# Kernel optimization log

Hardware: AMD Instinct MI355X
Metric: run time of the kernel (lower is better)

Reference implementation:

```python
import jax, jax.numpy as jnp
import numpy as np

NENTITY = 200000
NRELATION = 500
HIDDEN = 256
GAMMA = 12.0
EPS = 2.0
EMB_RANGE = (GAMMA + EPS) / HIDDEN


def setup_inputs() -> dict:
    key = jax.random.key(0)
    ks = jax.random.split(key, 8)
    B, NEG = 256, 1024
    head = jax.random.randint(ks[0], (B, 1), 0, NENTITY)
    tail = jax.random.randint(ks[1], (B, NEG), 0, NENTITY)
    relation = jax.random.randint(ks[2], (B,), 0, NRELATION)
    entity_emb = jax.random.uniform(ks[3], (NENTITY, HIDDEN), jnp.float32, -EMB_RANGE, EMB_RANGE)
    relation_emb = jax.random.uniform(ks[4], (NRELATION, 2 * HIDDEN), jnp.float32, -EMB_RANGE, EMB_RANGE)
    lim = 1.0 / np.sqrt(2 * HIDDEN)
    W_fc = jax.random.uniform(ks[5], (HIDDEN, 2 * HIDDEN), jnp.float32, -lim, lim)
    b_fc = jax.random.uniform(ks[6], (HIDDEN,), jnp.float32, -lim, lim)
    return {"head": head, "tail": tail, "relation": relation,
            "entity_emb": entity_emb, "relation_emb": relation_emb,
            "W_fc": W_fc, "b_fc": b_fc}


def _l2_normalize(x):
    # F.normalize(x, p=2, dim=-1): x / max(||x||_2, 1e-12)
    n = jnp.sqrt(jnp.sum(x * x, axis=-1, keepdims=True))
    return x / jnp.maximum(n, 1e-12)


def reference(head, tail, relation, entity_emb, relation_emb, W_fc, b_fc):
    # gather embeddings
    h = entity_emb[head]                      # [B, 1,   d]
    t = entity_emb[tail]                      # [B, NEG, d]
    r = relation_emb[relation][:, None, :]    # [B, 1, 2d]
    re_head, re_tail = jnp.split(r, 2, axis=-1)   # each [B, 1, d]
    # broadcast relation halves to match head/tail sample counts, then concat
    re_h = jnp.broadcast_to(re_head, h.shape)
    re_t = jnp.broadcast_to(re_tail, t.shape)
    h_cat = jnp.concatenate([h, re_h], axis=-1)   # [B, 1,   2d]
    t_cat = jnp.concatenate([t, re_t], axis=-1)   # [B, NEG, 2d]
    # shared small FC (torch Linear: x @ W^T + b)
    h_fc = jnp.einsum('bnk,dk->bnd', h_cat, W_fc) + b_fc
    t_fc = jnp.einsum('bnk,dk->bnd', t_cat, W_fc) + b_fc
    h_n = _l2_normalize(h_fc)
    t_n = _l2_normalize(t_fc)
    diff = h_n - t_n                              # [B, NEG, d]
    score = GAMMA - jnp.sum(jnp.abs(diff), axis=2)  # [B, NEG]
    return score
```

## Files before the change

kernel.cpp:

```cpp
#include <hip/hip_runtime.h>
#include <math.h>

#define NENTITY 200000
#define HIDDEN 256
#define NEG 1024
#define NBATCH 256
#define GAMMA_F 12.0f
#define BM 32
#define NTILES 8
#define NBLK 1024
#define CHUNK 128

typedef short v8s __attribute__((ext_vector_type(8)));
typedef float v4f __attribute__((ext_vector_type(4)));
typedef unsigned int u32;

#define LDS_BARRIER() asm volatile("s_waitcnt lgkmcnt(0)\n\ts_barrier" ::: "memory")

__device__ __forceinline__ short f2bf(float x) {
    u32 u = __float_as_uint(x);
    u = (u + 0x7fffu + ((u >> 16) & 1u)) >> 16;
    return (short)u;
}

__device__ __forceinline__ u32 rhu(float f) { return __float_as_uint(f) + 0x8000u; }
__device__ __forceinline__ v8s pack8(const float4& x0, const float4& x1) {
    int4 fr;
    fr.x = __builtin_amdgcn_perm(rhu(x0.y), rhu(x0.x), 0x07060302u);
    fr.y = __builtin_amdgcn_perm(rhu(x0.w), rhu(x0.z), 0x07060302u);
    fr.z = __builtin_amdgcn_perm(rhu(x1.y), rhu(x1.x), 0x07060302u);
    fr.w = __builtin_amdgcn_perm(rhu(x1.w), rhu(x1.z), 0x07060302u);
    return __builtin_bit_cast(v8s, fr);
}

__global__ __launch_bounds__(256) void prep_kernel(
    const int* __restrict__ head, const int* __restrict__ relation,
    const float* __restrict__ entity_emb, const float* __restrict__ relation_emb,
    const float* __restrict__ W_fc, const float* __restrict__ b_fc,
    short* __restrict__ W1bf, float* __restrict__ h_n, float* __restrict__ rel_part)
{
    const int b = blockIdx.x;
    const int t = threadIdx.x;

    W1bf[b * HIDDEN + t] = f2bf(W_fc[(size_t)b * 2 * HIDDEN + t]);

    __shared__ float xh[2 * HIDDEN];
    __shared__ float xt[HIDDEN];
    __shared__ float red[256];

    const int hidx = head[b];
    const int r = relation[b];
    xh[t]          = entity_emb[(size_t)hidx * HIDDEN + t];
    xh[HIDDEN + t] = relation_emb[(size_t)r * 2 * HIDDEN + t];
    xt[t]          = relation_emb[(size_t)r * 2 * HIDDEN + HIDDEN + t];
    __syncthreads();

    const float4* wrow = reinterpret_cast<const float4*>(W_fc + (size_t)t * 2 * HIDDEN);
    float hf = b_fc[t];
    float rp = b_fc[t];
    #pragma unroll 4
    for (int kk = 0; kk < HIDDEN / 4; ++kk) {
        float4 w = wrow[kk];
        hf += xh[4*kk+0]*w.x + xh[4*kk+1]*w.y + xh[4*kk+2]*w.z + xh[4*kk+3]*w.w;
    }
    #pragma unroll 4
    for (int kk = 0; kk < HIDDEN / 4; ++kk) {
        float4 w = wrow[HIDDEN/4 + kk];
        hf += xh[HIDDEN+4*kk+0]*w.x + xh[HIDDEN+4*kk+1]*w.y + xh[HIDDEN+4*kk+2]*w.z + xh[HIDDEN+4*kk+3]*w.w;
        rp += xt[4*kk+0]*w.x + xt[4*kk+1]*w.y + xt[4*kk+2]*w.z + xt[4*kk+3]*w.w;
    }
    rel_part[b * HIDDEN + t] = rp;

    red[t] = hf * hf;
    __syncthreads();
    for (int s = 128; s > 0; s >>= 1) {
        if (t < s) red[t] += red[t + s];
        __syncthreads();
    }
    const float norm = sqrtf(red[0]);
    h_n[b * HIDDEN + t] = hf / fmaxf(norm, 1e-12f);
}

__global__ __launch_bounds__(256, 2) void proj_kernel(
    const float* __restrict__ entity_emb, const short* __restrict__ W1bf,
    short* __restrict__ P)
{
    __shared__ __align__(16) float Asf[BM * HIDDEN];

    const int t = threadIdx.x;
    const int w = t >> 6;
    const int l = t & 63;
    const int c = t & 15;
    const int g = (t >> 4) & 3;
    const int R0 = blockIdx.x * BM;

    v8s Bf[4][8];
    #pragma unroll
    for (int ntl = 0; ntl < 4; ++ntl) {
        const short* bsrc = W1bf + (size_t)(64 * w + ntl * 16 + c) * HIDDEN + g * 8;
        #pragma unroll
        for (int kt = 0; kt < 8; ++kt)
            Bf[ntl][kt] = *reinterpret_cast<const v8s*>(bsrc + kt * 32);
    }
    #pragma unroll
    for (int ntl = 0; ntl < 4; ++ntl)
        #pragma unroll
        for (int kt = 0; kt < 8; ++kt)
            asm volatile("" : "+v"(Bf[ntl][kt]));

    v4f st[8];
    #pragma unroll
    for (int i = 0; i < 8; ++i) {
        const int r = w * 8 + i;
        st[i] = *reinterpret_cast<const v4f*>(
            entity_emb + (size_t)(R0 + r) * HIDDEN + (l << 2));
    }
    __builtin_amdgcn_sched_barrier(0);
    #pragma unroll
    for (int i = 0; i < 8; ++i) {
        const int r = w * 8 + i;
        *reinterpret_cast<v4f*>(&Asf[r * HIDDEN + ((l ^ (r & 7)) << 2)]) = st[i];
    }
    LDS_BARRIER();

    v4f acc[2][4];
    #pragma unroll
    for (int mt = 0; mt < 2; ++mt)
        #pragma unroll
        for (int ntl = 0; ntl < 4; ++ntl)
            acc[mt][ntl] = v4f{0.f, 0.f, 0.f, 0.f};

    const float* a0base = &Asf[c * HIDDEN];
    const float* a1base = &Asf[(16 + c) * HIDDEN];
    const int swz = c & 7;

    #pragma unroll
    for (int kt = 0; kt < 8; ++kt) {
        const int u0 = kt * 8 + g * 2;
        float4 x0 = *reinterpret_cast<const float4*>(a0base + (((u0    ) ^ swz) << 2));
        float4 x1 = *reinterpret_cast<const float4*>(a0base + (((u0 + 1) ^ swz) << 2));
        float4 y0 = *reinterpret_cast<const float4*>(a1base + (((u0    ) ^ swz) << 2));
        float4 y1 = *reinterpret_cast<const float4*>(a1base + (((u0 + 1) ^ swz) << 2));
        v8s a0 = pack8(x0, x1);
        v8s a1 = pack8(y0, y1);
        #pragma unroll
        for (int ntl = 0; ntl < 4; ++ntl) {
            acc[0][ntl] = __builtin_amdgcn_mfma_f32_16x16x32_bf16(a0, Bf[ntl][kt], acc[0][ntl], 0, 0, 0);
            acc[1][ntl] = __builtin_amdgcn_mfma_f32_16x16x32_bf16(a1, Bf[ntl][kt], acc[1][ntl], 0, 0, 0);
        }
    }

    #pragma unroll
    for (int mt = 0; mt < 2; ++mt)
        #pragma unroll
        for (int ntl = 0; ntl < 4; ++ntl)
            #pragma unroll
            for (int r = 0; r < 4; ++r) {
                const int m = mt * 16 + g * 4 + r;
                const int n = 64 * w + ntl * 16 + c;
                P[(size_t)(R0 + m) * HIDDEN + n] = f2bf(acc[mt][ntl][r]);
            }
}

__global__ __launch_bounds__(256) void score2_kernel(
    const int* __restrict__ tail, const short* __restrict__ P,
    const float* __restrict__ h_n, const float* __restrict__ rel_part,
    float* __restrict__ out)
{
    const int t = threadIdx.x;
    const int w = t >> 6;
    const int l = t & 63;
    const int b = blockIdx.x >> 3;
    const int chunk = blockIdx.x & 7;
    const int base = b * NEG + chunk * CHUNK;

    __shared__ int tl[CHUNK];
    if (t < CHUNK) tl[t] = tail[base + t];

    const float4 hh = *reinterpret_cast<const float4*>(h_n + b * HIDDEN + 4 * l);
    const float4 rp = *reinterpret_cast<const float4*>(rel_part + b * HIDDEN + 4 * l);
    __syncthreads();

    uint2 st2[8];
    #pragma unroll
    for (int i = 0; i < 8; ++i)
        st2[i] = *(reinterpret_cast<const uint2*>(P + (size_t)tl[w * 32 + i] * HIDDEN) + l);

    #pragma unroll
    for (int p = 0; p < 32; ++p) {
        uint2 v = st2[p & 7];
        if (p + 8 < 32)
            st2[p & 7] = *(reinterpret_cast<const uint2*>(
                P + (size_t)tl[w * 32 + p + 8] * HIDDEN) + l);

        float t0 = __uint_as_float(v.x << 16)          + rp.x;
        float t1 = __uint_as_float(v.x & 0xffff0000u)  + rp.y;
        float t2 = __uint_as_float(v.y << 16)          + rp.z;
        float t3 = __uint_as_float(v.y & 0xffff0000u)  + rp.w;

        float ssq = t0 * t0 + t1 * t1 + t2 * t2 + t3 * t3;
        #pragma unroll
        for (int mask = 1; mask < 64; mask <<= 1) ssq += __shfl_xor(ssq, mask);
        const float rn = 1.f / fmaxf(sqrtf(ssq), 1e-12f);

        float l1 = fabsf(hh.x - t0 * rn) + fabsf(hh.y - t1 * rn)
                 + fabsf(hh.z - t2 * rn) + fabsf(hh.w - t3 * rn);
        #pragma unroll
        for (int mask = 1; mask < 64; mask <<= 1) l1 += __shfl_xor(l1, mask);

        if (l == 0) out[base + w * 32 + p] = GAMMA_F - l1;
    }
}

__global__ __launch_bounds__(256, 2) void score_kernel(
    const int* __restrict__ tail, const float* __restrict__ entity_emb,
    const short* __restrict__ W1bf, const float* __restrict__ h_n,
    const float* __restrict__ rel_part, float* __restrict__ out)
{
    __shared__ __align__(16) float Asf[2][BM * HIDDEN];
    __shared__ int tails[NTILES * BM];
    __shared__ float ssq_lds[4][BM];
    __shared__ float l1_lds[4][BM];

    const int t = threadIdx.x;
    const int w = t >> 6;
    const int l = t & 63;
    const int c = t & 15;
    const int g = (t >> 4) & 3;
    const int b = blockIdx.x >> 2;

    tails[t] = tail[blockIdx.x * (NTILES * BM) + t];

    float rlv[4], hnv[4];
    #pragma unroll
    for (int ntl = 0; ntl < 4; ++ntl) {
        const int n = 64 * w + ntl * 16 + c;
        rlv[ntl] = rel_part[b * HIDDEN + n];
        hnv[ntl] = h_n[b * HIDDEN + n];
    }

    v8s Bf[4][8];
    #pragma unroll
    for (int ntl = 0; ntl < 4; ++ntl) {
        const short* bsrc = W1bf + (size_t)(64 * w + ntl * 16 + c) * HIDDEN + g * 8;
        #pragma unroll
        for (int kt = 0; kt < 8; ++kt)
            Bf[ntl][kt] = *reinterpret_cast<const v8s*>(bsrc + kt * 32);
    }

    __syncthreads();

    v4f st[8];
    auto issue = [&](int j) {
        #pragma unroll
        for (int i = 0; i < 8; ++i) {
            const int r = w * 8 + i;
            const float* src = entity_emb + (size_t)tails[j * BM + r] * HIDDEN + (l << 2);
            st[i] = *reinterpret_cast<const v4f*>(src);
        }
        __builtin_amdgcn_sched_barrier(0);
    };
    auto commit = [&](int buf) {
        #pragma unroll
        for (int i = 0; i < 8; ++i) {
            const int r = w * 8 + i;
            *reinterpret_cast<v4f*>(&Asf[buf][r * HIDDEN + ((l ^ (r & 7)) << 2)]) = st[i];
        }
    };

    issue(0);
    commit(0);
    LDS_BARRIER();

    #pragma unroll 1
    for (int j = 0; j < NTILES; ++j) {
        const int cur = j & 1;
        if (j + 1 < NTILES) issue(j + 1);

        v4f acc[2][4];
        #pragma unroll
        for (int mt = 0; mt < 2; ++mt)
            #pragma unroll
            for (int ntl = 0; ntl < 4; ++ntl)
                acc[mt][ntl] = v4f{0.f, 0.f, 0.f, 0.f};

        const float* a0base = &Asf[cur][c * HIDDEN];
        const float* a1base = &Asf[cur][(16 + c) * HIDDEN];
        const int swz = c & 7;

        #pragma unroll
        for (int kt = 0; kt < 8; ++kt) {
            const int u0 = kt * 8 + g * 2;
            float4 x0 = *reinterpret_cast<const float4*>(a0base + (((u0    ) ^ swz) << 2));
            float4 x1 = *reinterpret_cast<const float4*>(a0base + (((u0 + 1) ^ swz) << 2));
            float4 y0 = *reinterpret_cast<const float4*>(a1base + (((u0    ) ^ swz) << 2));
            float4 y1 = *reinterpret_cast<const float4*>(a1base + (((u0 + 1) ^ swz) << 2));
            v8s a0 = pack8(x0, x1);
            v8s a1 = pack8(y0, y1);
            #pragma unroll
            for (int ntl = 0; ntl < 4; ++ntl) {
                acc[0][ntl] = __builtin_amdgcn_mfma_f32_16x16x32_bf16(a0, Bf[ntl][kt], acc[0][ntl], 0, 0, 0);
                acc[1][ntl] = __builtin_amdgcn_mfma_f32_16x16x32_bf16(a1, Bf[ntl][kt], acc[1][ntl], 0, 0, 0);
            }
        }

        #pragma unroll
        for (int mt = 0; mt < 2; ++mt) {
            float ssq[4] = {0.f, 0.f, 0.f, 0.f};
            #pragma unroll
            for (int ntl = 0; ntl < 4; ++ntl) {
                #pragma unroll
                for (int r = 0; r < 4; ++r) {
                    float tf = acc[mt][ntl][r] + rlv[ntl];
                    acc[mt][ntl][r] = tf;
                    ssq[r] += tf * tf;
                }
            }
            #pragma unroll
            for (int mask = 1; mask < 16; mask <<= 1) {
                #pragma unroll
                for (int r = 0; r < 4; ++r) ssq[r] += __shfl_xor(ssq[r], mask);
            }
            if (c == 0) {
                #pragma unroll
                for (int r = 0; r < 4; ++r) ssq_lds[w][mt * 16 + g * 4 + r] = ssq[r];
            }
        }
        LDS_BARRIER();

        #pragma unroll
        for (int mt = 0; mt < 2; ++mt) {
            float rn[4], s1[4] = {0.f, 0.f, 0.f, 0.f};
            #pragma unroll
            for (int r = 0; r < 4; ++r) {
                const int m = mt * 16 + g * 4 + r;
                float tot = ssq_lds[0][m] + ssq_lds[1][m] + ssq_lds[2][m] + ssq_lds[3][m];
                rn[r] = 1.f / fmaxf(sqrtf(tot), 1e-12f);
            }
            #pragma unroll
            for (int ntl = 0; ntl < 4; ++ntl) {
                #pragma unroll
                for (int r = 0; r < 4; ++r)
                    s1[r] += fabsf(hnv[ntl] - acc[mt][ntl][r] * rn[r]);
            }
            #pragma unroll
            for (int mask = 1; mask < 16; mask <<= 1) {
                #pragma unroll
                for (int r = 0; r < 4; ++r) s1[r] += __shfl_xor(s1[r], mask);
            }
            if (c == 0) {
                #pragma unroll
                for (int r = 0; r < 4; ++r) l1_lds[w][mt * 16 + g * 4 + r] = s1[r];
            }
        }

        if (j + 1 < NTILES) commit(cur ^ 1);
        LDS_BARRIER();

        if (t < BM) {
            out[blockIdx.x * (NTILES * BM) + j * BM + t] = GAMMA_F -
                (l1_lds[0][t] + l1_lds[1][t] + l1_lds[2][t] + l1_lds[3][t]);
        }
    }
}

extern "C" void kernel_launch(void* const* d_in, const int* in_sizes, int n_in,
                              void* d_out, int out_size, void* d_ws, size_t ws_size,
                              hipStream_t stream)
{
    const int*   head         = (const int*)d_in[0];
    const int*   tail         = (const int*)d_in[1];
    const int*   relation     = (const int*)d_in[2];
    const float* entity_emb   = (const float*)d_in[3];
    const float* relation_emb = (const float*)d_in[4];
    const float* W_fc         = (const float*)d_in[5];
    const float* b_fc         = (const float*)d_in[6];
    float* out = (float*)d_out;

    short* W1bf     = (short*)d_ws;
    float* h_n      = (float*)((char*)d_ws + 131072);
    float* rel_part = (float*)((char*)d_ws + 131072 + 262144);

    prep_kernel<<<NBATCH, 256, 0, stream>>>(head, relation, entity_emb, relation_emb,
                                            W_fc, b_fc, W1bf, h_n, rel_part);

    const size_t P_OFF   = 1ull << 20;
    const size_t P_BYTES = (size_t)NENTITY * HIDDEN * sizeof(short);
    if (ws_size >= P_OFF + P_BYTES) {
        short* P = (short*)((char*)d_ws + P_OFF);
        proj_kernel<<<NENTITY / BM, 256, 0, stream>>>(entity_emb, W1bf, P);
        score2_kernel<<<NBATCH * 8, 256, 0, stream>>>(tail, P, h_n, rel_part, out);
    } else {
        score_kernel<<<NBLK, 256, 0, stream>>>(tail, entity_emb, W1bf,
                                               h_n, rel_part, out);
    }
}
```

Before: 413.0 us.

## Make projection kernel persistent over 8 tiles with double-buffered LDS prefetch

Each projection block now processes eight 32-row entity tiles instead of one. The W fragments are loaded once per block, and the next tile's global loads are issued while the current tile's MFMAs run, using a double-buffered LDS. The MFMA operand order is swapped so each lane holds 4 consecutive output columns, which allows packed 8-byte bf16 stores instead of scalar 2-byte stores. The grid shrinks about 8x, so there are fewer blocks to hide latency with, and the doubled LDS use may lower occupancy.

```diff
diff --git a/kernel.cpp b/kernel.cpp
--- a/kernel.cpp
+++ b/kernel.cpp
@@ -9,6 +9,7 @@
 #define BM 32
 #define NTILES 8
 #define NBLK 1024
+#define NT_P 8
 #define CHUNK 128
 
 typedef short v8s __attribute__((ext_vector_type(8)));
@@ -85,81 +86,103 @@
     const float* __restrict__ entity_emb, const short* __restrict__ W1bf,
     short* __restrict__ P)
 {
-    __shared__ __align__(16) float Asf[BM * HIDDEN];
+    __shared__ __align__(16) float Asf[2][BM * HIDDEN];
 
     const int t = threadIdx.x;
     const int w = t >> 6;
     const int l = t & 63;
     const int c = t & 15;
     const int g = (t >> 4) & 3;
-    const int R0 = blockIdx.x * BM;
-
-    v8s Bf[4][8];
-    #pragma unroll
-    for (int ntl = 0; ntl < 4; ++ntl) {
-        const short* bsrc = W1bf + (size_t)(64 * w + ntl * 16 + c) * HIDDEN + g * 8;
+    const int E0 = blockIdx.x * (NT_P * BM);
+
+    v8s Wf[4][8];
+    #pragma unroll
+    for (int f = 0; f < 4; ++f) {
+        const short* bsrc = W1bf + (size_t)(64 * w + f * 16 + c) * HIDDEN + g * 8;
         #pragma unroll
         for (int kt = 0; kt < 8; ++kt)
-            Bf[ntl][kt] = *reinterpret_cast<const v8s*>(bsrc + kt * 32);
-    }
-    #pragma unroll
-    for (int ntl = 0; ntl < 4; ++ntl)
+            Wf[f][kt] = *reinterpret_cast<const v8s*>(bsrc + kt * 32);
+    }
+    #pragma unroll
+    for (int f = 0; f < 4; ++f)
         #pragma unroll
         for (int kt = 0; kt < 8; ++kt)
-            asm volatile("" : "+v"(Bf[ntl][kt]));
+            asm volatile("" : "+v"(Wf[f][kt]));
 
     v4f st[8];
-    #pragma unroll
-    for (int i = 0; i < 8; ++i) {
-        const int r = w * 8 + i;
-        st[i] = *reinterpret_cast<const v4f*>(
-            entity_emb + (size_t)(R0 + r) * HIDDEN + (l << 2));
-    }
-    __builtin_amdgcn_sched_barrier(0);
-    #pragma unroll
-    for (int i = 0; i < 8; ++i) {
-        const int r = w * 8 + i;
-        *reinterpret_cast<v4f*>(&Asf[r * HIDDEN + ((l ^ (r & 7)) << 2)]) = st[i];
-    }
+    auto issue = [&](int j) {
+        #pragma unroll
+        for (int i = 0; i < 8; ++i) {
+            int row = E0 + j * BM + w * 8 + i;
+            row = row < NENTITY ? row : NENTITY - 1;
+            st[i] = *reinterpret_cast<const v4f*>(
+                entity_emb + (size_t)row * HIDDEN + (l << 2));
+        }
+        __builtin_amdgcn_sched_barrier(0);
+    };
+    auto commit = [&](int buf) {
+        #pragma unroll
+        for (int i = 0; i < 8; ++i) {
+            const int r = w * 8 + i;
+            *reinterpret_cast<v4f*>(&Asf[buf][r * HIDDEN + ((l ^ (r & 7)) << 2)]) = st[i];
+        }
+    };
+
+    issue(0);
+    commit(0);
     LDS_BARRIER();
 
-    v4f acc[2][4];
-    #pragma unroll
-    for (int mt = 0; mt < 2; ++mt)
-        #pragma unroll
-        for (int ntl = 0; ntl < 4; ++ntl)
-            acc[mt][ntl] = v4f{0.f, 0.f, 0.f, 0.f};
-
-    const float* a0base = &Asf[c * HIDDEN];
-    const float* a1base = &Asf[(16 + c) * HIDDEN];
-    const int swz = c & 7;
-
-    #pragma unroll
-    for (int kt = 0; kt < 8; ++kt) {
-        const int u0 = kt * 8 + g * 2;
-        float4 x0 = *reinterpret_cast<const float4*>(a0base + (((u0    ) ^ swz) << 2));
-        float4 x1 = *reinterpret_cast<const float4*>(a0base + (((u0 + 1) ^ swz) << 2));
-        float4 y0 = *reinterpret_cast<const float4*>(a1base + (((u0    ) ^ swz) << 2));
-        float4 y1 = *reinterpret_cast<const float4*>(a1base + (((u0 + 1) ^ swz) << 2));
-        v8s a0 = pack8(x0, x1);
-        v8s a1 = pack8(y0, y1);
-        #pragma unroll
-        for (int ntl = 0; ntl < 4; ++ntl) {
-            acc[0][ntl] = __builtin_amdgcn_mfma_f32_16x16x32_bf16(a0, Bf[ntl][kt], acc[0][ntl], 0, 0, 0);
-            acc[1][ntl] = __builtin_amdgcn_mfma_f32_16x16x32_bf16(a1, Bf[ntl][kt], acc[1][ntl], 0, 0, 0);
-        }
-    }
-
-    #pragma unroll
-    for (int mt = 0; mt < 2; ++mt)
-        #pragma unroll
-        for (int ntl = 0; ntl < 4; ++ntl)
-            #pragma unroll
-            for (int r = 0; r < 4; ++r) {
-                const int m = mt * 16 + g * 4 + r;
-                const int n = 64 * w + ntl * 16 + c;
-                P[(size_t)(R0 + m) * HIDDEN + n] = f2bf(acc[mt][ntl][r]);
-            }
+    #pragma unroll 1
+    for (int j = 0; j < NT_P; ++j) {
+        const int cur = j & 1;
+        if (j + 1 < NT_P) issue(j + 1);
+
+        v4f acc[4][2];
+        #pragma unroll
+        for (int f = 0; f < 4; ++f)
+            #pragma unroll
+            for (int et = 0; et < 2; ++et)
+                acc[f][et] = v4f{0.f, 0.f, 0.f, 0.f};
+
+        const float* a0base = &Asf[cur][c * HIDDEN];
+        const float* a1base = &Asf[cur][(16 + c) * HIDDEN];
+        const int swz = c & 7;
+
+        #pragma unroll
+        for (int kt = 0; kt < 8; ++kt) {
+            const int u0 = kt * 8 + g * 2;
+            float4 x0 = *reinterpret_cast<const float4*>(a0base + (((u0    ) ^ swz) << 2));
+            float4 x1 = *reinterpret_cast<const float4*>(a0base + (((u0 + 1) ^ swz) << 2));
+            float4 y0 = *reinterpret_cast<const float4*>(a1base + (((u0    ) ^ swz) << 2));
+            float4 y1 = *reinterpret_cast<const float4*>(a1base + (((u0 + 1) ^ swz) << 2));
+            v8s e0 = pack8(x0, x1);
+            v8s e1 = pack8(y0, y1);
+            #pragma unroll
+            for (int f = 0; f < 4; ++f) {
+                acc[f][0] = __builtin_amdgcn_mfma_f32_16x16x32_bf16(Wf[f][kt], e0, acc[f][0], 0, 0, 0);
+                acc[f][1] = __builtin_amdgcn_mfma_f32_16x16x32_bf16(Wf[f][kt], e1, acc[f][1], 0, 0, 0);
+            }
+        }
+
+        if (j + 1 < NT_P) commit(cur ^ 1);
+
+        #pragma unroll
+        for (int et = 0; et < 2; ++et) {
+            const int e = E0 + j * BM + et * 16 + c;
+            if (e < NENTITY) {
+                short* dst = P + (size_t)e * HIDDEN + 64 * w + g * 4;
+                #pragma unroll
+                for (int f = 0; f < 4; ++f) {
+                    uint2 pk;
+                    pk.x = __builtin_amdgcn_perm(rhu(acc[f][et][1]), rhu(acc[f][et][0]), 0x07060302u);
+                    pk.y = __builtin_amdgcn_perm(rhu(acc[f][et][3]), rhu(acc[f][et][2]), 0x07060302u);
+                    *reinterpret_cast<uint2*>(dst + f * 16) = pk;
+                }
+            }
+        }
+
+        LDS_BARRIER();
+    }
 }
 
 __global__ __launch_bounds__(256) void score2_kernel(
@@ -388,7 +411,8 @@
     const size_t P_BYTES = (size_t)NENTITY * HIDDEN * sizeof(short);
     if (ws_size >= P_OFF + P_BYTES) {
         short* P = (short*)((char*)d_ws + P_OFF);
-        proj_kernel<<<NENTITY / BM, 256, 0, stream>>>(entity_emb, W1bf, P);
+        const int grid = (NENTITY + NT_P * BM - 1) / (NT_P * BM);
+        proj_kernel<<<grid, 256, 0, stream>>>(entity_emb, W1bf, P);
         score2_kernel<<<NBATCH * 8, 256, 0, stream>>>(tail, P, h_n, rel_part, out);
     } else {
         score_kernel<<<NBLK, 256, 0, stream>>>(tail, entity_emb, W1bf,
```

After: 390.5 us. 5.4% less time.
